# Performance work log

Measured on AMD Instinct MI355X. Metric: run time of the kernel, lower is better.

Reference implementation:

```python
import jax, jax.numpy as jnp
import numpy as np

N, D_IN, D_OUT = 8192, 1024, 1024

def setup_inputs() -> dict:
    key = jax.random.key(0)
    kx, kq, kk, kv = jax.random.split(key, 4)
    s = 1.0 / np.sqrt(D_IN)
    return {
        "x": jax.random.normal(kx, (N, D_IN), dtype=jnp.float32),
        "W_q": jax.random.normal(kq, (D_OUT, D_IN), dtype=jnp.float32) * s,
        "W_k": jax.random.normal(kk, (D_OUT, D_IN), dtype=jnp.float32) * s,
        "W_v": jax.random.normal(kv, (D_OUT, D_IN), dtype=jnp.float32) * s,
    }

def reference(x, W_q, W_k, W_v):
    # nn.Linear stores weight as [out, in]: y = x @ W.T
    q = x @ W_q.T          # [N, D_OUT]
    k = x @ W_k.T          # [N, D_OUT]
    v = x @ W_v.T          # [N, D_OUT]
    scale = 1.0 / jnp.sqrt(jnp.asarray(k.shape[-1], dtype=x.dtype))
    scores = (q @ k.T) * scale            # [N, N]
    attn = jax.nn.softmax(scores, axis=-1)
    return attn @ v                        # [N, D_OUT]
```

## Files before the change

kernel.cpp:

```cpp
#include <hip/hip_runtime.h>
#include <hip/hip_bf16.h>
#include <cstdint>
#include <cstddef>


typedef __attribute__((ext_vector_type(8))) short short8;
typedef __attribute__((ext_vector_type(8))) unsigned short ushort8;
typedef __attribute__((ext_vector_type(4))) float f32x4;

#define FENCE asm volatile("" ::: "memory")

__device__ __forceinline__ unsigned short f2bf(float f) {
  unsigned u = __float_as_uint(f);
  u += 0x7fffu + ((u >> 16) & 1u);
  return (unsigned short)(u >> 16);
}
__device__ __forceinline__ float bf2f(unsigned short h) {
  return __uint_as_float(((unsigned)h) << 16);
}

__device__ __forceinline__ void glds16(const void* g, void* l) {
  __builtin_amdgcn_global_load_lds((__attribute__((address_space(1))) void*)g,
                                   (__attribute__((address_space(3))) void*)l,
                                   16, 0, 0);
}

__global__ __launch_bounds__(256) void cast_kernel(const float* __restrict__ in,
                                                   unsigned short* __restrict__ out,
                                                   int n8) {
  int i = blockIdx.x * 256 + threadIdx.x;
  if (i >= n8) return;
  const f32x4* in4 = (const f32x4*)in;
  f32x4 a = in4[2 * i];
  f32x4 b = in4[2 * i + 1];
  ushort8 o;
#pragma unroll
  for (int j = 0; j < 4; ++j) o[j] = f2bf(a[j]);
#pragma unroll
  for (int j = 0; j < 4; ++j) o[4 + j] = f2bf(b[j]);
  ((ushort8*)out)[i] = o;
}

#define MFMA_OP(mi, ni, av, bv) \
  acc[mi][ni] = __builtin_amdgcn_mfma_f32_16x16x32_bf16(av, bv, acc[mi][ni], 0, 0, 0)

template <typename OutT>
__device__ __forceinline__ void gemm_core(
    const unsigned short* __restrict__ A, const unsigned short* __restrict__ B,
    OutT* __restrict__ C, int ldc, size_t ldab , int NT,
    int gm0, int gn0, float scale, char* lA, char* lB) {
  const int tid = threadIdx.x;
  const int lane = tid & 63, w = tid >> 6;
  const int wm = w >> 2, wn = w & 3;

  const int rc0 = w * 32 + (lane >> 2);
  const int rc1 = rc0 + 16;
  const int scol = ((lane & 3) << 4) ^ (((lane >> 3) & 3) << 4);
  const char* pA0 = (const char*)A + (size_t)(gm0 + rc0) * ldab + scol;
  const char* pA1 = (const char*)A + (size_t)(gm0 + rc1) * ldab + scol;
  const char* pB0 = (const char*)B + (size_t)(gn0 + rc0) * ldab + scol;
  const char* pB1 = (const char*)B + (size_t)(gn0 + rc1) * ldab + scol;
  char* dA = lA + w * 2048;
  char* dB = lB + w * 2048;

  const int colb = ((lane >> 4) << 4) ^ (((lane >> 1) & 3) << 4);
  const int aoff = (wm * 128 + (lane & 15)) * 64 + colb;
  const int boff = (wn * 64 + (lane & 15)) * 64 + colb;

  f32x4 acc[8][4];
#pragma unroll
  for (int m = 0; m < 8; ++m)
#pragma unroll
    for (int n = 0; n < 4; ++n) acc[m][n] = (f32x4)(0.0f);

  for (int t = 0; t < 2; ++t) {
    glds16(pA0 + (size_t)t * 64, dA + t * 16384);
    glds16(pA1 + (size_t)t * 64, dA + t * 16384 + 1024);
    glds16(pB0 + (size_t)t * 64, dB + t * 16384);
    glds16(pB1 + (size_t)t * 64, dB + t * 16384 + 1024);
  }
  asm volatile("s_waitcnt vmcnt(4)" ::: "memory");
  __builtin_amdgcn_s_barrier();
  FENCE;

  const char* sA0 = pA0 + 128;
  const char* sA1 = pA1 + 128;
  const char* sB0 = pB0 + 128;
  const char* sB1 = pB1 + 128;

#pragma unroll 4
  for (int t = 0; t < NT; ++t) {
    const int slot = t & 3;
    const char* As = lA + slot * 16384;
    const char* Bs = lB + slot * 16384;
    const bool stg = (t + 2 < NT);
    const int s2 = (t + 2) & 3;
    short8 a0, a1, a2, a3, b0, b1, b2, b3;

    if (stg) {
      glds16(sA0, dA + s2 * 16384);
      glds16(sA1, dA + s2 * 16384 + 1024);
    }
    a0 = *(const short8*)(As + aoff);
    a1 = *(const short8*)(As + aoff + 1024);
    a2 = *(const short8*)(As + aoff + 2048);
    a3 = *(const short8*)(As + aoff + 3072);
    b0 = *(const short8*)(Bs + boff);
    b1 = *(const short8*)(Bs + boff + 1024);
    b2 = *(const short8*)(Bs + boff + 2048);
    b3 = *(const short8*)(Bs + boff + 3072);
    __builtin_amdgcn_s_setprio(1);
    MFMA_OP(0, 0, a0, b0); MFMA_OP(0, 1, a0, b1);
    MFMA_OP(0, 2, a0, b2); MFMA_OP(0, 3, a0, b3);
    MFMA_OP(1, 0, a1, b0); MFMA_OP(1, 1, a1, b1);
    MFMA_OP(1, 2, a1, b2); MFMA_OP(1, 3, a1, b3);
    MFMA_OP(2, 0, a2, b0); MFMA_OP(2, 1, a2, b1);
    MFMA_OP(2, 2, a2, b2); MFMA_OP(2, 3, a2, b3);
    MFMA_OP(3, 0, a3, b0); MFMA_OP(3, 1, a3, b1);
    MFMA_OP(3, 2, a3, b2); MFMA_OP(3, 3, a3, b3);
    __builtin_amdgcn_s_setprio(0);

    if (stg) {
      glds16(sB0, dB + s2 * 16384);
      glds16(sB1, dB + s2 * 16384 + 1024);
    }
    sA0 += 64; sA1 += 64; sB0 += 64; sB1 += 64;

    a0 = *(const short8*)(As + aoff + 4096);
    a1 = *(const short8*)(As + aoff + 5120);
    a2 = *(const short8*)(As + aoff + 6144);
    a3 = *(const short8*)(As + aoff + 7168);
    __builtin_amdgcn_s_setprio(1);
    MFMA_OP(4, 0, a0, b0); MFMA_OP(4, 1, a0, b1);
    MFMA_OP(4, 2, a0, b2); MFMA_OP(4, 3, a0, b3);
    MFMA_OP(5, 0, a1, b0); MFMA_OP(5, 1, a1, b1);
    MFMA_OP(5, 2, a1, b2); MFMA_OP(5, 3, a1, b3);
    MFMA_OP(6, 0, a2, b0); MFMA_OP(6, 1, a2, b1);
    MFMA_OP(6, 2, a2, b2); MFMA_OP(6, 3, a2, b3);
    MFMA_OP(7, 0, a3, b0); MFMA_OP(7, 1, a3, b1);
    MFMA_OP(7, 2, a3, b2); MFMA_OP(7, 3, a3, b3);
    __builtin_amdgcn_s_setprio(0);

    if (stg) asm volatile("s_waitcnt vmcnt(4)" ::: "memory");
    else     asm volatile("s_waitcnt vmcnt(0)" ::: "memory");
    __builtin_amdgcn_s_barrier();
    FENCE;
  }

  const int r0 = gm0 + wm * 128 + ((lane >> 4) << 2);
  const int c0 = gn0 + wn * 64 + (lane & 15);
#pragma unroll
  for (int mi = 0; mi < 8; ++mi) {
#pragma unroll
    for (int ni = 0; ni < 4; ++ni) {
      f32x4 v = acc[mi][ni];
#pragma unroll
      for (int j = 0; j < 4; ++j) {
        float val = v[j] * scale;
        size_t idx = (size_t)(r0 + mi * 16 + j) * ldc + (c0 + ni * 16);
        if (sizeof(OutT) == 2) ((unsigned short*)C)[idx] = f2bf(val);
        else                   ((float*)C)[idx] = val;
      }
    }
  }
}

__device__ __forceinline__ void swz_block(int& bx, int& by, int& bz) {
  const int gx = gridDim.x, gy = gridDim.y;
  const int f = (blockIdx.z * gy + blockIdx.y) * gx + blockIdx.x;
  const int nwg = gx * gy * gridDim.z;
  const int q = nwg >> 3;
  const int l = (f & 7) * q + (f >> 3);
  bx = l % gx;
  const int r = l / gx;
  by = r % gy;
  bz = r / gy;
}

__global__ __launch_bounds__(512, 2) void gemm_s_kernel(
    const unsigned short* __restrict__ Q, const unsigned short* __restrict__ Kh,
    unsigned short* __restrict__ S) {
  __shared__ char lA[4 * 16384];
  __shared__ char lB[4 * 16384];
  int bx, by, bz; swz_block(bx, by, bz);
  gemm_core<unsigned short>(Q, Kh, S, 8192, 2048, 32, by * 256, bx * 256,
                            0.03125f, lA, lB);
}

__global__ __launch_bounds__(512, 2) void gemm_qkv_kernel(
    const unsigned short* __restrict__ X,
    const unsigned short* __restrict__ Wq, const unsigned short* __restrict__ Wk,
    const unsigned short* __restrict__ Wv,
    unsigned short* __restrict__ Qo, unsigned short* __restrict__ Ko,
    unsigned short* __restrict__ Vo) {
  __shared__ char lA[4 * 16384];
  __shared__ char lB[4 * 16384];
  int bx, by, bz; swz_block(bx, by, bz);
  const unsigned short* B = (bz == 0) ? Wq : (bz == 1) ? Wk : Wv;
  unsigned short* C = (bz == 0) ? Qo : (bz == 1) ? Ko : Vo;
  gemm_core<unsigned short>(X, B, C, 1024, 2048, 32, by * 256, bx * 256,
                            1.0f, lA, lB);
}

__global__ __launch_bounds__(512, 2) void gemm_pv_kernel(
    const unsigned short* __restrict__ S, const unsigned short* __restrict__ Vt,
    float* __restrict__ O, float* __restrict__ P1) {
  __shared__ char lA[4 * 16384];
  __shared__ char lB[4 * 16384];
  int bx, by, bz; swz_block(bx, by, bz);
  const unsigned short* A = S + (size_t)bz * 4096;
  const unsigned short* B = Vt + (size_t)bz * 4096;
  float* C = bz ? P1 : O;
  gemm_core<float>(A, B, C, 1024, 16384, 128, by * 256, bx * 256, 1.0f, lA, lB);
}

__global__ __launch_bounds__(256) void add_kernel(float* __restrict__ out,
                                                  const float* __restrict__ p,
                                                  int n4) {
  int i = blockIdx.x * 256 + threadIdx.x;
  if (i < n4) {
    f32x4 a = ((const f32x4*)out)[i];
    f32x4 b = ((const f32x4*)p)[i];
    ((f32x4*)out)[i] = a + b;
  }
}

__global__ __launch_bounds__(256) void softmax_kernel(unsigned short* __restrict__ S,
                                                      int ncol) {
  const int t = threadIdx.x;
  unsigned short* rp = S + (size_t)blockIdx.x * ncol;
  ushort8* rv = (ushort8*)rp;
  float f[32];
#pragma unroll
  for (int c = 0; c < 4; ++c) {
    ushort8 v = rv[c * 256 + t];
#pragma unroll
    for (int j = 0; j < 8; ++j) f[c * 8 + j] = bf2f(v[j]);
  }
  float m = -1e30f;
#pragma unroll
  for (int i = 0; i < 32; ++i) m = fmaxf(m, f[i]);
#pragma unroll
  for (int o = 32; o; o >>= 1) m = fmaxf(m, __shfl_xor(m, o));
  __shared__ float red[8];
  if ((t & 63) == 0) red[t >> 6] = m;
  __syncthreads();
  m = fmaxf(fmaxf(red[0], red[1]), fmaxf(red[2], red[3]));

  float s = 0.0f;
#pragma unroll
  for (int i = 0; i < 32; ++i) {
    f[i] = __expf(f[i] - m);
    s += f[i];
  }
#pragma unroll
  for (int o = 32; o; o >>= 1) s += __shfl_xor(s, o);
  if ((t & 63) == 0) red[4 + (t >> 6)] = s;
  __syncthreads();
  s = red[4] + red[5] + red[6] + red[7];
  float inv = 1.0f / s;
#pragma unroll
  for (int c = 0; c < 4; ++c) {
    ushort8 v;
#pragma unroll
    for (int j = 0; j < 8; ++j) v[j] = f2bf(f[c * 8 + j] * inv);
    rv[c * 256 + t] = v;
  }
}

__global__ __launch_bounds__(256) void transpose_kernel(
    const unsigned short* __restrict__ in, unsigned short* __restrict__ out,
    int R, int Ccols) {
  __shared__ unsigned short tile[64][65];
  const int tx = threadIdx.x & 63, ty = threadIdx.x >> 6;
  const int r0 = blockIdx.y * 64, c0 = blockIdx.x * 64;
#pragma unroll
  for (int i = 0; i < 16; ++i) {
    int r = ty * 16 + i;
    tile[r][tx] = in[(size_t)(r0 + r) * Ccols + c0 + tx];
  }
  __syncthreads();
#pragma unroll
  for (int i = 0; i < 16; ++i) {
    int r = ty * 16 + i;
    out[(size_t)(c0 + r) * R + r0 + tx] = tile[tx][r];
  }
}

extern "C" void kernel_launch(void* const* d_in, const int* in_sizes, int n_in,
                              void* d_out, int out_size, void* d_ws, size_t ws_size,
                              hipStream_t stream) {
  (void)in_sizes; (void)n_in; (void)out_size; (void)ws_size;
  const int N = 8192, D = 1024;
  const float* x  = (const float*)d_in[0];
  const float* Wq = (const float*)d_in[1];
  const float* Wk = (const float*)d_in[2];
  const float* Wv = (const float*)d_in[3];
  float* out = (float*)d_out;

  char* ws = (char*)d_ws;
  size_t off = 0;
  auto alloc = [&](size_t bytes) { char* p = ws + off; off += bytes; return p; };
  unsigned short* xh  = (unsigned short*)alloc((size_t)N * D * 2);
  unsigned short* Wqh = (unsigned short*)alloc((size_t)D * D * 2);
  unsigned short* Wkh = (unsigned short*)alloc((size_t)D * D * 2);
  unsigned short* Wvh = (unsigned short*)alloc((size_t)D * D * 2);
  unsigned short* Qh  = (unsigned short*)alloc((size_t)N * D * 2);
  unsigned short* Kh  = (unsigned short*)alloc((size_t)N * D * 2);
  unsigned short* Vh  = (unsigned short*)alloc((size_t)N * D * 2);
  unsigned short* S   = (unsigned short*)alloc((size_t)N * N * 2);
  unsigned short* Vth = xh;
  float* Pbuf = (float*)Qh;

  cast_kernel<<<(N * D / 8) / 256, 256, 0, stream>>>(x, xh, N * D / 8);
  cast_kernel<<<(D * D / 8) / 256, 256, 0, stream>>>(Wq, Wqh, D * D / 8);
  cast_kernel<<<(D * D / 8) / 256, 256, 0, stream>>>(Wk, Wkh, D * D / 8);
  cast_kernel<<<(D * D / 8) / 256, 256, 0, stream>>>(Wv, Wvh, D * D / 8);

  gemm_qkv_kernel<<<dim3(4, 32, 3), 512, 0, stream>>>(xh, Wqh, Wkh, Wvh,
                                                      Qh, Kh, Vh);

  gemm_s_kernel<<<dim3(32, 32), 512, 0, stream>>>(Qh, Kh, S);

  softmax_kernel<<<N, 256, 0, stream>>>(S, N);

  transpose_kernel<<<dim3(D / 64, N / 64), 256, 0, stream>>>(Vh, Vth, N, D);

  gemm_pv_kernel<<<dim3(4, 32, 2), 512, 0, stream>>>(S, Vth, out, Pbuf);

  add_kernel<<<(N * D / 4) / 256, 256, 0, stream>>>(out, Pbuf, N * D / 4);
}
```

Measured before the change: 505.6 us.

## Shrink GEMM tiles to 128x128 with 256 threads and double-buffered LDS

Changes the shared GEMM core from 256x256 tiles with 512 threads and a 4-slot, two-ahead LDS pipeline to 128x128 tiles with 256 threads (2x2 waves of 64x64) and a simple two-slot double buffer. Grids quadruple and launch bounds move to 4 blocks per CU, aiming for more parallelism and smaller LDS and register footprints. In exchange, each tile reuses its loaded data less, global traffic per flop roughly doubles, and the prefetch depth drops from two stages to one, with a full vmcnt(0) wait every iteration.

```diff
diff --git a/kernel.cpp b/kernel.cpp
--- a/kernel.cpp
+++ b/kernel.cpp
@@ -48,109 +48,81 @@
 __device__ __forceinline__ void gemm_core(
     const unsigned short* __restrict__ A, const unsigned short* __restrict__ B,
     OutT* __restrict__ C, int ldc, size_t ldab , int NT,
-    int gm0, int gn0, float scale, char* lA, char* lB) {
+    int gm0, int gn0, float scale, char* lds) {
   const int tid = threadIdx.x;
-  const int lane = tid & 63, w = tid >> 6;
-  const int wm = w >> 2, wn = w & 3;
-
-  const int rc0 = w * 32 + (lane >> 2);
-  const int rc1 = rc0 + 16;
-  const int scol = ((lane & 3) << 4) ^ (((lane >> 3) & 3) << 4);
-  const char* pA0 = (const char*)A + (size_t)(gm0 + rc0) * ldab + scol;
-  const char* pA1 = (const char*)A + (size_t)(gm0 + rc1) * ldab + scol;
-  const char* pB0 = (const char*)B + (size_t)(gn0 + rc0) * ldab + scol;
-  const char* pB1 = (const char*)B + (size_t)(gn0 + rc1) * ldab + scol;
-  char* dA = lA + w * 2048;
-  char* dB = lB + w * 2048;
+  const int lane = tid & 63;
+  const int wm = (tid >> 7) & 1, wn = (tid >> 6) & 1;
+
+  const int srow = tid >> 2;
+  const int scol = ((tid & 3) << 4) ^ (((tid >> 3) & 3) << 4);
+  const char* pA0 = (const char*)A + (size_t)(gm0 + srow) * ldab + scol;
+  const char* pA1 = pA0 + (size_t)64 * ldab;
+  const char* pB0 = (const char*)B + (size_t)(gn0 + srow) * ldab + scol;
+  const char* pB1 = pB0 + (size_t)64 * ldab;
+  const int dst = tid * 16;
 
   const int colb = ((lane >> 4) << 4) ^ (((lane >> 1) & 3) << 4);
-  const int aoff = (wm * 128 + (lane & 15)) * 64 + colb;
-  const int boff = (wn * 64 + (lane & 15)) * 64 + colb;
-
-  f32x4 acc[8][4];
-#pragma unroll
-  for (int m = 0; m < 8; ++m)
+  const int aoff = (wm * 64 + (lane & 15)) * 64 + colb;
+  const int boff = (wn * 64 + (lane & 15)) * 64 + colb + 8192;
+
+  f32x4 acc[4][4];
+#pragma unroll
+  for (int m = 0; m < 4; ++m)
 #pragma unroll
     for (int n = 0; n < 4; ++n) acc[m][n] = (f32x4)(0.0f);
 
-  for (int t = 0; t < 2; ++t) {
-    glds16(pA0 + (size_t)t * 64, dA + t * 16384);
-    glds16(pA1 + (size_t)t * 64, dA + t * 16384 + 1024);
-    glds16(pB0 + (size_t)t * 64, dB + t * 16384);
-    glds16(pB1 + (size_t)t * 64, dB + t * 16384 + 1024);
-  }
-  asm volatile("s_waitcnt vmcnt(4)" ::: "memory");
+  glds16(pA0, lds + dst);
+  glds16(pA1, lds + 4096 + dst);
+  glds16(pB0, lds + 8192 + dst);
+  glds16(pB1, lds + 12288 + dst);
+  asm volatile("s_waitcnt vmcnt(0)" ::: "memory");
   __builtin_amdgcn_s_barrier();
   FENCE;
 
-  const char* sA0 = pA0 + 128;
-  const char* sA1 = pA1 + 128;
-  const char* sB0 = pB0 + 128;
-  const char* sB1 = pB1 + 128;
-
-#pragma unroll 4
+  const char* sA0 = pA0 + 64;
+  const char* sA1 = pA1 + 64;
+  const char* sB0 = pB0 + 64;
+  const char* sB1 = pB1 + 64;
+
+#pragma unroll 2
   for (int t = 0; t < NT; ++t) {
-    const int slot = t & 3;
-    const char* As = lA + slot * 16384;
-    const char* Bs = lB + slot * 16384;
-    const bool stg = (t + 2 < NT);
-    const int s2 = (t + 2) & 3;
-    short8 a0, a1, a2, a3, b0, b1, b2, b3;
+    const char* Ls = lds + (t & 1) * 16384;
+    char* Ld = lds + ((t + 1) & 1) * 16384;
+    const bool stg = (t + 1 < NT);
 
     if (stg) {
-      glds16(sA0, dA + s2 * 16384);
-      glds16(sA1, dA + s2 * 16384 + 1024);
+      glds16(sA0, Ld + dst);
+      glds16(sA1, Ld + 4096 + dst);
+      glds16(sB0, Ld + 8192 + dst);
+      glds16(sB1, Ld + 12288 + dst);
+      sA0 += 64; sA1 += 64; sB0 += 64; sB1 += 64;
     }
-    a0 = *(const short8*)(As + aoff);
-    a1 = *(const short8*)(As + aoff + 1024);
-    a2 = *(const short8*)(As + aoff + 2048);
-    a3 = *(const short8*)(As + aoff + 3072);
-    b0 = *(const short8*)(Bs + boff);
-    b1 = *(const short8*)(Bs + boff + 1024);
-    b2 = *(const short8*)(Bs + boff + 2048);
-    b3 = *(const short8*)(Bs + boff + 3072);
+
+    short8 aF[4], bF[4];
+#pragma unroll
+    for (int m = 0; m < 4; ++m)
+      aF[m] = *(const short8*)(Ls + aoff + m * 1024);
+#pragma unroll
+    for (int n = 0; n < 4; ++n)
+      bF[n] = *(const short8*)(Ls + boff + n * 1024);
+
     __builtin_amdgcn_s_setprio(1);
-    MFMA_OP(0, 0, a0, b0); MFMA_OP(0, 1, a0, b1);
-    MFMA_OP(0, 2, a0, b2); MFMA_OP(0, 3, a0, b3);
-    MFMA_OP(1, 0, a1, b0); MFMA_OP(1, 1, a1, b1);
-    MFMA_OP(1, 2, a1, b2); MFMA_OP(1, 3, a1, b3);
-    MFMA_OP(2, 0, a2, b0); MFMA_OP(2, 1, a2, b1);
-    MFMA_OP(2, 2, a2, b2); MFMA_OP(2, 3, a2, b3);
-    MFMA_OP(3, 0, a3, b0); MFMA_OP(3, 1, a3, b1);
-    MFMA_OP(3, 2, a3, b2); MFMA_OP(3, 3, a3, b3);
+#pragma unroll
+    for (int m = 0; m < 4; ++m) {
+      MFMA_OP(m, 0, aF[m], bF[0]); MFMA_OP(m, 1, aF[m], bF[1]);
+      MFMA_OP(m, 2, aF[m], bF[2]); MFMA_OP(m, 3, aF[m], bF[3]);
+    }
     __builtin_amdgcn_s_setprio(0);
 
-    if (stg) {
-      glds16(sB0, dB + s2 * 16384);
-      glds16(sB1, dB + s2 * 16384 + 1024);
-    }
-    sA0 += 64; sA1 += 64; sB0 += 64; sB1 += 64;
-
-    a0 = *(const short8*)(As + aoff + 4096);
-    a1 = *(const short8*)(As + aoff + 5120);
-    a2 = *(const short8*)(As + aoff + 6144);
-    a3 = *(const short8*)(As + aoff + 7168);
-    __builtin_amdgcn_s_setprio(1);
-    MFMA_OP(4, 0, a0, b0); MFMA_OP(4, 1, a0, b1);
-    MFMA_OP(4, 2, a0, b2); MFMA_OP(4, 3, a0, b3);
-    MFMA_OP(5, 0, a1, b0); MFMA_OP(5, 1, a1, b1);
-    MFMA_OP(5, 2, a1, b2); MFMA_OP(5, 3, a1, b3);
-    MFMA_OP(6, 0, a2, b0); MFMA_OP(6, 1, a2, b1);
-    MFMA_OP(6, 2, a2, b2); MFMA_OP(6, 3, a2, b3);
-    MFMA_OP(7, 0, a3, b0); MFMA_OP(7, 1, a3, b1);
-    MFMA_OP(7, 2, a3, b2); MFMA_OP(7, 3, a3, b3);
-    __builtin_amdgcn_s_setprio(0);
-
-    if (stg) asm volatile("s_waitcnt vmcnt(4)" ::: "memory");
-    else     asm volatile("s_waitcnt vmcnt(0)" ::: "memory");
+    asm volatile("s_waitcnt vmcnt(0)" ::: "memory");
     __builtin_amdgcn_s_barrier();
     FENCE;
   }
 
-  const int r0 = gm0 + wm * 128 + ((lane >> 4) << 2);
+  const int r0 = gm0 + wm * 64 + ((lane >> 4) << 2);
   const int c0 = gn0 + wn * 64 + (lane & 15);
 #pragma unroll
-  for (int mi = 0; mi < 8; ++mi) {
+  for (int mi = 0; mi < 4; ++mi) {
 #pragma unroll
     for (int ni = 0; ni < 4; ++ni) {
       f32x4 v = acc[mi][ni];
@@ -177,41 +149,38 @@
   bz = r / gy;
 }
 
-__global__ __launch_bounds__(512, 2) void gemm_s_kernel(
+__global__ __launch_bounds__(256, 4) void gemm_s_kernel(
     const unsigned short* __restrict__ Q, const unsigned short* __restrict__ Kh,
     unsigned short* __restrict__ S) {
-  __shared__ char lA[4 * 16384];
-  __shared__ char lB[4 * 16384];
+  __shared__ char lds[2 * 16384];
   int bx, by, bz; swz_block(bx, by, bz);
-  gemm_core<unsigned short>(Q, Kh, S, 8192, 2048, 32, by * 256, bx * 256,
-                            0.03125f, lA, lB);
-}
-
-__global__ __launch_bounds__(512, 2) void gemm_qkv_kernel(
+  gemm_core<unsigned short>(Q, Kh, S, 8192, 2048, 32, by * 128, bx * 128,
+                            0.03125f, lds);
+}
+
+__global__ __launch_bounds__(256, 4) void gemm_qkv_kernel(
     const unsigned short* __restrict__ X,
     const unsigned short* __restrict__ Wq, const unsigned short* __restrict__ Wk,
     const unsigned short* __restrict__ Wv,
     unsigned short* __restrict__ Qo, unsigned short* __restrict__ Ko,
     unsigned short* __restrict__ Vo) {
-  __shared__ char lA[4 * 16384];
-  __shared__ char lB[4 * 16384];
+  __shared__ char lds[2 * 16384];
   int bx, by, bz; swz_block(bx, by, bz);
   const unsigned short* B = (bz == 0) ? Wq : (bz == 1) ? Wk : Wv;
   unsigned short* C = (bz == 0) ? Qo : (bz == 1) ? Ko : Vo;
-  gemm_core<unsigned short>(X, B, C, 1024, 2048, 32, by * 256, bx * 256,
-                            1.0f, lA, lB);
-}
-
-__global__ __launch_bounds__(512, 2) void gemm_pv_kernel(
+  gemm_core<unsigned short>(X, B, C, 1024, 2048, 32, by * 128, bx * 128,
+                            1.0f, lds);
+}
+
+__global__ __launch_bounds__(256, 4) void gemm_pv_kernel(
     const unsigned short* __restrict__ S, const unsigned short* __restrict__ Vt,
     float* __restrict__ O, float* __restrict__ P1) {
-  __shared__ char lA[4 * 16384];
-  __shared__ char lB[4 * 16384];
+  __shared__ char lds[2 * 16384];
   int bx, by, bz; swz_block(bx, by, bz);
   const unsigned short* A = S + (size_t)bz * 4096;
   const unsigned short* B = Vt + (size_t)bz * 4096;
   float* C = bz ? P1 : O;
-  gemm_core<float>(A, B, C, 1024, 16384, 128, by * 256, bx * 256, 1.0f, lA, lB);
+  gemm_core<float>(A, B, C, 1024, 16384, 128, by * 128, bx * 128, 1.0f, lds);
 }
 
 __global__ __launch_bounds__(256) void add_kernel(float* __restrict__ out,
@@ -317,16 +286,16 @@
   cast_kernel<<<(D * D / 8) / 256, 256, 0, stream>>>(Wk, Wkh, D * D / 8);
   cast_kernel<<<(D * D / 8) / 256, 256, 0, stream>>>(Wv, Wvh, D * D / 8);
 
-  gemm_qkv_kernel<<<dim3(4, 32, 3), 512, 0, stream>>>(xh, Wqh, Wkh, Wvh,
+  gemm_qkv_kernel<<<dim3(8, 64, 3), 256, 0, stream>>>(xh, Wqh, Wkh, Wvh,
                                                       Qh, Kh, Vh);
 
-  gemm_s_kernel<<<dim3(32, 32), 512, 0, stream>>>(Qh, Kh, S);
+  gemm_s_kernel<<<dim3(64, 64), 256, 0, stream>>>(Qh, Kh, S);
 
   softmax_kernel<<<N, 256, 0, stream>>>(S, N);
 
   transpose_kernel<<<dim3(D / 64, N / 64), 256, 0, stream>>>(Vh, Vth, N, D);
 
-  gemm_pv_kernel<<<dim3(4, 32, 2), 512, 0, stream>>>(S, Vth, out, Pbuf);
+  gemm_pv_kernel<<<dim3(8, 64, 2), 256, 0, stream>>>(S, Vth, out, Pbuf);
 
   add_kernel<<<(N * D / 4) / 256, 256, 0, stream>>>(out, Pbuf, N * D / 4);
 }
```

Result: slower. 553.0 us (+9.4%).
